# Kernel optimization log

Hardware: AMD Instinct MI355X
Metric: run time of the kernel (lower is better)

## Reference

```python
import jax, jax.numpy as jnp
import numpy as np

B, S, D, H = 4, 2048, 1024, 16
DH = D // H
NEG = -1e9


def setup_inputs() -> dict:
    key = jax.random.key(0)
    ks = jax.random.split(key, 6)
    return {
        "q_raw": jax.random.normal(ks[0], (B, S, D), jnp.float32),
        "kv_raw": jax.random.normal(ks[1], (B, S, D), jnp.float32),
        "padding_mask": jnp.ones((B, S), jnp.int32),
        "Wq": jax.random.normal(ks[2], (D, D), jnp.float32) * 0.02,
        "Wk": jax.random.normal(ks[3], (D, D), jnp.float32) * 0.02,
        "Wv": jax.random.normal(ks[4], (D, D), jnp.float32) * 0.02,
        "Wo": jax.random.normal(ks[5], (D, D), jnp.float32) * 0.02,
    }


def _split_heads(x):
    # (B, S, D) -> (B, H, S, DH)
    return x.reshape(B, S, H, DH).transpose(0, 2, 1, 3)


def reference(q_raw, kv_raw, padding_mask, Wq, Wk, Wv, Wo):
    # nn.Linear (no bias): y = x @ W.T
    q = _split_heads(q_raw @ Wq.T)
    k = _split_heads(kv_raw @ Wk.T)
    v = _split_heads(kv_raw @ Wv.T)

    scale = 1.0 / jnp.sqrt(jnp.float32(DH))
    scores = jnp.einsum("bhqd,bhkd->bhqk", q, k) * scale  # (B,H,S,S)

    # padding mask: 0 -> masked (broadcast over query dim), as in torch code
    pad = (padding_mask == 0)[:, None, None, :]  # (B,1,1,S)
    scores = jnp.where(pad, NEG, scores)
    # causal mask (only applied when padding_mask given, matching original)
    causal = jnp.triu(jnp.ones((S, S), bool), k=1)  # (S,S)
    scores = jnp.where(causal[None, None], NEG, scores)

    w = jax.nn.softmax(scores, axis=-1)
    att = jnp.einsum("bhqk,bhkd->bhqd", w, v)  # (B,H,S,DH)
    att = att.transpose(0, 2, 1, 3).reshape(B, S, D)
    return att @ Wo.T
```

## Files before the change

kernel.cpp:

```cpp
#include <hip/hip_runtime.h>
#include <stdint.h>

typedef __attribute__((ext_vector_type(8))) short  short8;
typedef __attribute__((ext_vector_type(4))) float  f32x4;
typedef __attribute__((ext_vector_type(4))) unsigned short us4;

static __device__ __forceinline__ unsigned short f2bf(float x) {
  unsigned u = __builtin_bit_cast(unsigned, x);
  u += 0x7FFFu + ((u >> 16) & 1u);
  return (unsigned short)(u >> 16);
}

static __device__ __forceinline__ unsigned cvt_pk_bf16(float lo, float hi) {
  unsigned r;
  asm("v_cvt_pk_bf16_f32 %0, %1, %2" : "=v"(r) : "v"(lo), "v"(hi));
  return r;
}

template <int CTRL>
static __device__ __forceinline__ float maxdpp(float v) {
  int o = __builtin_amdgcn_update_dpp(0, __builtin_bit_cast(int, v), CTRL, 0xf, 0xf, false);
  return fmaxf(v, __builtin_bit_cast(float, o));
}
static __device__ __forceinline__ float rowmax16(float v) {
  v = maxdpp<0xB1>(v);
  v = maxdpp<0x4E>(v);
  v = maxdpp<0x141>(v);
  v = maxdpp<0x140>(v);
  return v;
}

__global__ __launch_bounds__(256) void cvt6(const float* __restrict__ q_raw,
                                            const float* __restrict__ kv_raw,
                                            const float* __restrict__ Wq,
                                            const float* __restrict__ Wk,
                                            const float* __restrict__ Wv,
                                            const float* __restrict__ Wo,
                                            unsigned short* __restrict__ qbf,
                                            unsigned short* __restrict__ kvbf,
                                            unsigned short* __restrict__ wbf) {
  const int y = blockIdx.y;
  const float* in;
  unsigned short* out;
  int n4;
  if (y == 0)      { in = q_raw;  out = qbf;  n4 = 2097152; }
  else if (y == 1) { in = kv_raw; out = kvbf; n4 = 2097152; }
  else {
    in  = (y == 2) ? Wq : (y == 3) ? Wk : (y == 4) ? Wv : Wo;
    out = wbf + (size_t)(y - 2) * 1048576;
    n4 = 262144;
  }
  int i = blockIdx.x * 256 + threadIdx.x;
  const int stride = gridDim.x * 256;
  for (; i < n4; i += stride) {
    f32x4 v = *((const f32x4*)in + i);
    us4 o = { f2bf(v[0]), f2bf(v[1]), f2bf(v[2]), f2bf(v[3]) };
    *((us4*)out + i) = o;
  }
}

__global__ __launch_bounds__(1024) void bias_kernel(const int* __restrict__ pm,
                                                    float* __restrict__ bias,
                                                    unsigned* __restrict__ flagmask) {
  __shared__ unsigned m;
  const int b = blockIdx.x, tid = threadIdx.x;
  if (tid == 0) m = 0;
  __syncthreads();
  const int i0 = b * 2048 + tid;
  const int z0 = pm[i0], z1 = pm[i0 + 1024];
  bias[i0]        = z0 ? 0.f : -1.0e9f;
  bias[i0 + 1024] = z1 ? 0.f : -1.0e9f;
  const int wv = tid >> 6;
  unsigned long long b0 = __ballot(z0 == 0);
  unsigned long long b1 = __ballot(z1 == 0);
  if ((tid & 63) == 0) {
    unsigned bits = (b0 ? (1u << wv) : 0u) | (b1 ? (1u << (wv + 16)) : 0u);
    if (bits) atomicOr(&m, bits);
  }
  __syncthreads();
  if (tid == 0) flagmask[b] = m;
}

static __device__ __forceinline__ void g2l16(const void* g, void* l) {
  __builtin_amdgcn_global_load_lds(
      (const __attribute__((address_space(1))) void*)g,
      (__attribute__((address_space(3))) void*)l, 16, 0, 0);
}

__global__ __launch_bounds__(256) void gemm_proj(const unsigned short* __restrict__ qbf,
                                                 const unsigned short* __restrict__ kvbf,
                                                 const unsigned short* __restrict__ wbf,
                                                 unsigned short* __restrict__ Qp,
                                                 unsigned short* __restrict__ Kp,
                                                 unsigned short* __restrict__ Vtp,
                                                 float qscale) {
  __shared__ unsigned short Alds[2][4096];
  __shared__ unsigned short Blds[2][4096];
  const int tid  = threadIdx.x;
  const int lane = tid & 63;
  const int w    = tid >> 6;
  const int g    = lane >> 4;
  const int li   = lane & 15;

  const int l = blockIdx.x;
  const int xcd = l & 7, j = l >> 3;
  const int mstep = j & 7, rn = j >> 3;
  const int region = rn >> 3;
  const int n0 = (rn & 7) * 128;
  const int m0 = (xcd * 8 + mstep) * 128;
  const int wm = (w >> 1) * 64;
  const int wn = (w & 1) * 64;

  const unsigned short* A = (region == 0) ? qbf : kvbf;
  const unsigned short* W = wbf + (size_t)region * 1048576;

  int aoff[4], boff[4];
#pragma unroll
  for (int mi = 0; mi < 4; ++mi) {
    int row = wm + mi * 16 + li;
    aoff[mi] = row * 32 + (g ^ ((row >> 1) & 3)) * 8;
  }
#pragma unroll
  for (int ni = 0; ni < 4; ++ni) {
    int col = wn + ni * 16 + li;
    boff[ni] = col * 32 + (g ^ ((col >> 1) & 3)) * 8;
  }

  const int s1 = tid, s2 = 256 + tid;
  const int r1 = s1 >> 2, gc1 = (s1 & 3) ^ ((r1 >> 1) & 3);
  const int r2 = s2 >> 2, gc2 = (s2 & 3) ^ ((r2 >> 1) & 3);
  const unsigned short* gA1 = A + (size_t)(m0 + r1) * 1024 + gc1 * 8;
  const unsigned short* gA2 = A + (size_t)(m0 + r2) * 1024 + gc2 * 8;
  const unsigned short* gB1 = W + (size_t)(n0 + r1) * 1024 + gc1 * 8;
  const unsigned short* gB2 = W + (size_t)(n0 + r2) * 1024 + gc2 * 8;

  f32x4 acc[4][4] = {};

  g2l16(gA1, &Alds[0][w * 512]); g2l16(gA2, &Alds[0][2048 + w * 512]);
  g2l16(gB1, &Blds[0][w * 512]); g2l16(gB2, &Blds[0][2048 + w * 512]);
  gA1 += 32; gA2 += 32; gB1 += 32; gB2 += 32;

  int cur = 0;
#pragma unroll 1
  for (int kt = 0; kt < 32; ++kt) {
    if (kt < 31) {
      g2l16(gA1, &Alds[cur ^ 1][w * 512]); g2l16(gA2, &Alds[cur ^ 1][2048 + w * 512]);
      g2l16(gB1, &Blds[cur ^ 1][w * 512]); g2l16(gB2, &Blds[cur ^ 1][2048 + w * 512]);
      gA1 += 32; gA2 += 32; gB1 += 32; gB2 += 32;
      asm volatile("s_waitcnt vmcnt(4)" ::: "memory");
    } else {
      asm volatile("s_waitcnt vmcnt(0)" ::: "memory");
    }
    __builtin_amdgcn_s_barrier();
    short8 af[4], bf[4];
#pragma unroll
    for (int mi = 0; mi < 4; ++mi) af[mi] = *(const short8*)&Alds[cur][aoff[mi]];
#pragma unroll
    for (int ni = 0; ni < 4; ++ni) bf[ni] = *(const short8*)&Blds[cur][boff[ni]];
#pragma unroll
    for (int mi = 0; mi < 4; ++mi)
#pragma unroll
      for (int ni = 0; ni < 4; ++ni)
        acc[mi][ni] = __builtin_amdgcn_mfma_f32_16x16x32_bf16(af[mi], bf[ni], acc[mi][ni], 0, 0, 0);
    __builtin_amdgcn_s_barrier();
    cur ^= 1;
  }

  if (region == 2) {
#pragma unroll
    for (int mi = 0; mi < 4; ++mi) {
      int mb = m0 + wm + mi * 16 + g * 4;
      int bb = mb >> 11, s = mb & 2047;
#pragma unroll
      for (int ni = 0; ni < 4; ++ni) {
        int n = n0 + wn + ni * 16 + li;
        us4 pk = { f2bf(acc[mi][ni][0]), f2bf(acc[mi][ni][1]),
                   f2bf(acc[mi][ni][2]), f2bf(acc[mi][ni][3]) };
        *(us4*)&Vtp[(size_t)(bb * 1024 + n) * 2048 + s] = pk;
      }
    }
  } else {
    unsigned short* C = (region == 0) ? Qp : Kp;
    const float sc = (region == 0) ? qscale : 1.0f;
#pragma unroll
    for (int mi = 0; mi < 4; ++mi) {
      int mb = m0 + wm + mi * 16 + g * 4;
#pragma unroll
      for (int ni = 0; ni < 4; ++ni) {
        int n = n0 + wn + ni * 16 + li;
#pragma unroll
        for (int r = 0; r < 4; ++r)
          C[(size_t)(mb + r) * 1024 + n] = f2bf(acc[mi][ni][r] * sc);
      }
    }
  }
}

__global__ __launch_bounds__(256) void gemm_out(const unsigned short* __restrict__ A,
                                                const unsigned short* __restrict__ W,
                                                float* __restrict__ C) {
  __shared__ unsigned short Alds[2][4096];
  __shared__ unsigned short Blds[2][4096];
  const int tid  = threadIdx.x;
  const int lane = tid & 63;
  const int w    = tid >> 6;
  const int g    = lane >> 4;
  const int li   = lane & 15;

  const int l = blockIdx.x;
  const int xcd = l & 7, j = l >> 3;
  const int mstep = j & 7, nt = j >> 3;
  const int m0 = (xcd * 8 + mstep) * 128;
  const int n0 = nt * 128;
  const int wm = (w >> 1) * 64;
  const int wn = (w & 1) * 64;

  int aoff[4], boff[4];
#pragma unroll
  for (int mi = 0; mi < 4; ++mi) {
    int row = wm + mi * 16 + li;
    aoff[mi] = row * 32 + (g ^ ((row >> 1) & 3)) * 8;
  }
#pragma unroll
  for (int ni = 0; ni < 4; ++ni) {
    int col = wn + ni * 16 + li;
    boff[ni] = col * 32 + (g ^ ((col >> 1) & 3)) * 8;
  }

  const int s1 = tid, s2 = 256 + tid;
  const int r1 = s1 >> 2, gc1 = (s1 & 3) ^ ((r1 >> 1) & 3);
  const int r2 = s2 >> 2, gc2 = (s2 & 3) ^ ((r2 >> 1) & 3);
  const unsigned short* gA1 = A + (size_t)(m0 + r1) * 1024 + gc1 * 8;
  const unsigned short* gA2 = A + (size_t)(m0 + r2) * 1024 + gc2 * 8;
  const unsigned short* gB1 = W + (size_t)(n0 + r1) * 1024 + gc1 * 8;
  const unsigned short* gB2 = W + (size_t)(n0 + r2) * 1024 + gc2 * 8;

  f32x4 acc[4][4] = {};

  g2l16(gA1, &Alds[0][w * 512]); g2l16(gA2, &Alds[0][2048 + w * 512]);
  g2l16(gB1, &Blds[0][w * 512]); g2l16(gB2, &Blds[0][2048 + w * 512]);
  gA1 += 32; gA2 += 32; gB1 += 32; gB2 += 32;

  int cur = 0;
#pragma unroll 1
  for (int kt = 0; kt < 32; ++kt) {
    if (kt < 31) {
      g2l16(gA1, &Alds[cur ^ 1][w * 512]); g2l16(gA2, &Alds[cur ^ 1][2048 + w * 512]);
      g2l16(gB1, &Blds[cur ^ 1][w * 512]); g2l16(gB2, &Blds[cur ^ 1][2048 + w * 512]);
      gA1 += 32; gA2 += 32; gB1 += 32; gB2 += 32;
      asm volatile("s_waitcnt vmcnt(4)" ::: "memory");
    } else {
      asm volatile("s_waitcnt vmcnt(0)" ::: "memory");
    }
    __builtin_amdgcn_s_barrier();
    short8 af[4], bf[4];
#pragma unroll
    for (int mi = 0; mi < 4; ++mi) af[mi] = *(const short8*)&Alds[cur][aoff[mi]];
#pragma unroll
    for (int ni = 0; ni < 4; ++ni) bf[ni] = *(const short8*)&Blds[cur][boff[ni]];
#pragma unroll
    for (int mi = 0; mi < 4; ++mi)
#pragma unroll
      for (int ni = 0; ni < 4; ++ni)
        acc[mi][ni] = __builtin_amdgcn_mfma_f32_16x16x32_bf16(af[mi], bf[ni], acc[mi][ni], 0, 0, 0);
    __builtin_amdgcn_s_barrier();
    cur ^= 1;
  }

#pragma unroll
  for (int mi = 0; mi < 4; ++mi) {
    int mb = m0 + wm + mi * 16 + g * 4;
#pragma unroll
    for (int ni = 0; ni < 4; ++ni) {
      int n = n0 + wn + ni * 16 + li;
#pragma unroll
      for (int r = 0; r < 4; ++r)
        C[(size_t)(mb + r) * 1024 + n] = acc[mi][ni][r];
    }
  }
}

__global__ __launch_bounds__(256, 4) void attn_kernel(const unsigned short* __restrict__ Qp,
                                                      const unsigned short* __restrict__ Kp,
                                                      const unsigned short* __restrict__ Vt,
                                                      const float* __restrict__ bias,
                                                      const unsigned* __restrict__ flagmask,
                                                      unsigned short* __restrict__ att) {
  __shared__ unsigned short Klds[2][64 * 64];
  __shared__ unsigned short Vlds[2][64 * 64];
  __shared__ unsigned short Plds[4][16 * 64];

  const int tid = threadIdx.x, lane = tid & 63, w = tid >> 6;
  const int g = lane >> 4, li = lane & 15;

  const int rid = blockIdx.x + (blockIdx.y << 4);
  const int xcd = rid & 7, kk = rid >> 3;
  const int bh = (kk & 7) | (xcd << 3);
  const int b = bh >> 4, h = bh & 15;
  const int tA = kk >> 3, tB = 31 - tA;
  const int nA = tA + 1, nB = tB + 1;

  const unsigned smask = flagmask[b];

  const int s1 = tid, s2 = tid + 256;
  const int r1 = s1 >> 3, c1 = (s1 & 7) ^ (r1 & 7);
  const int r2 = s2 >> 3, c2 = (s2 & 7) ^ (r2 & 7);
  const unsigned short* Kb1 = Kp + (size_t)(b * 2048 + r1) * 1024 + h * 64 + c1 * 8;
  const unsigned short* Kb2 = Kp + (size_t)(b * 2048 + r2) * 1024 + h * 64 + c2 * 8;
  const unsigned short* Vb1 = Vt + (size_t)(b * 1024 + h * 64 + r1) * 2048 + c1 * 8;
  const unsigned short* Vb2 = Vt + (size_t)(b * 1024 + h * 64 + r2) * 2048 + c2 * 8;

  int foff[2][4];
#pragma unroll
  for (int ks = 0; ks < 2; ++ks)
#pragma unroll
    for (int i = 0; i < 4; ++i)
      foff[ks][i] = (i * 16 + li) * 64 + (((ks * 4 + g) ^ (li & 7)) * 8);

  unsigned short* Pl = &Plds[w][0];
  const int swr = (li & 7) ^ (li >> 3);
  int poff[2];
#pragma unroll
  for (int ks = 0; ks < 2; ++ks) poff[ks] = li * 64 + ((ks * 4 + g) ^ swr) * 8;

  const float* bbase = bias + b * 2048 + li;

  short8 ones;
#pragma unroll
  for (int j2 = 0; j2 < 8; ++j2) ones[j2] = (short)0x3F80;

  int qw = tA * 64 + w * 16;
  short8 qfr[2];
#pragma unroll
  for (int ks = 0; ks < 2; ++ks)
    qfr[ks] = *(const short8*)&Qp[((size_t)(b * 2048 + qw + li)) * 1024 +
                                  h * 64 + ks * 32 + g * 8];

  f32x4 acco[4] = {};
  f32x4 lacc = {};
  float mrow[4] = {-3.0e38f, -3.0e38f, -3.0e38f, -3.0e38f};
  const f32x4 Z = {0.f, 0.f, 0.f, 0.f};

  auto stage = [&](int kt, int bufn) {
    const size_t ko = (size_t)kt * 65536, vo = (size_t)kt * 64;
    g2l16(Kb1 + ko, &Klds[bufn][w * 512]);
    g2l16(Kb2 + ko, &Klds[bufn][2048 + w * 512]);
    g2l16(Vb1 + vo, &Vlds[bufn][w * 512]);
    g2l16(Vb2 + vo, &Vlds[bufn][2048 + w * 512]);
  };

  auto body = [&](int kt, bool diag, int buf) {
    f32x4 s[4];
#pragma unroll
    for (int ni = 0; ni < 4; ++ni) {
      short8 kf = *(const short8*)&Klds[buf][foff[0][ni]];
      s[ni] = __builtin_amdgcn_mfma_f32_16x16x32_bf16(qfr[0], kf, Z, 0, 0, 0);
    }
#pragma unroll
    for (int ni = 0; ni < 4; ++ni) {
      short8 kf = *(const short8*)&Klds[buf][foff[1][ni]];
      s[ni] = __builtin_amdgcn_mfma_f32_16x16x32_bf16(qfr[1], kf, s[ni], 0, 0, 0);
    }
    if ((smask >> kt) & 1u) {
#pragma unroll
      for (int ni = 0; ni < 4; ++ni) {
        float bv = bbase[kt * 64 + ni * 16];
#pragma unroll
        for (int r = 0; r < 4; ++r) s[ni][r] += bv;
      }
    }
    if (diag) {
      const int q0 = qw + g * 4;
#pragma unroll
      for (int ni = 0; ni < 4; ++ni) {
        const int key = kt * 64 + ni * 16 + li;
#pragma unroll
        for (int r = 0; r < 4; ++r)
          if (key > q0 + r) s[ni][r] = -1.0e9f;
      }
    }
    float tm[4];
#pragma unroll
    for (int r = 0; r < 4; ++r)
      tm[r] = rowmax16(fmaxf(fmaxf(s[0][r], s[1][r]), fmaxf(s[2][r], s[3][r])));
    int need = 0;
#pragma unroll
    for (int r = 0; r < 4; ++r) need |= (tm[r] > mrow[r] + 8.0f) ? 1 : 0;
    if (__any(need)) {
#pragma unroll
      for (int r = 0; r < 4; ++r) {
        const float mn = fmaxf(mrow[r], tm[r]);
        const float al = __builtin_amdgcn_exp2f(mrow[r] - mn);
        mrow[r] = mn;
        lacc[r] *= al;
#pragma unroll
        for (int df = 0; df < 4; ++df) acco[df][r] *= al;
      }
    }
#pragma unroll
    for (int ni = 0; ni < 4; ++ni) {
#pragma unroll
      for (int h2 = 0; h2 < 2; ++h2) {
        float lo = __builtin_amdgcn_exp2f(s[ni][2 * h2]     - mrow[2 * h2]);
        float hi = __builtin_amdgcn_exp2f(s[ni][2 * h2 + 1] - mrow[2 * h2 + 1]);
        unsigned pk = cvt_pk_bf16(lo, hi);
        const int r0 = g * 4 + 2 * h2;
        const int ch = 2 * ni + (li >> 3);
        const int lo7 = li & 7;
        Pl[r0 * 64 + ((ch ^ ((r0 & 7) ^ (g >> 1))) * 8) + lo7] = (unsigned short)pk;
        const int rr = r0 + 1;
        Pl[rr * 64 + ((ch ^ ((rr & 7) ^ (g >> 1))) * 8) + lo7] = (unsigned short)(pk >> 16);
      }
    }
#pragma unroll
    for (int ks = 0; ks < 2; ++ks) {
      const short8 pa = *(const short8*)&Pl[poff[ks]];
      short8 vf[4];
#pragma unroll
      for (int df = 0; df < 4; ++df) vf[df] = *(const short8*)&Vlds[buf][foff[ks][df]];
#pragma unroll
      for (int df = 0; df < 4; ++df)
        acco[df] = __builtin_amdgcn_mfma_f32_16x16x32_bf16(pa, vf[df], acco[df], 0, 0, 0);
      lacc = __builtin_amdgcn_mfma_f32_16x16x32_bf16(pa, ones, lacc, 0, 0, 0);
    }
  };

  auto epilogue = [&]() {
    float inv[4];
#pragma unroll
    for (int r = 0; r < 4; ++r) inv[r] = __builtin_amdgcn_rcpf(lacc[r]);
    const int qb0 = qw + g * 4;
#pragma unroll
    for (int df = 0; df < 4; ++df) {
      const int d = h * 64 + df * 16 + li;
#pragma unroll
      for (int r = 0; r < 4; ++r)
        att[(size_t)(b * 2048 + qb0 + r) * 1024 + d] = f2bf(acco[df][r] * inv[r]);
    }
  };

  stage(0, 0);
  int buf = 0;

#pragma unroll 1
  for (int kt = 0; kt < nA; ++kt) {
    stage((kt + 1 < nA) ? kt + 1 : 0, buf ^ 1);
    asm volatile("s_waitcnt vmcnt(4)" ::: "memory");
    __builtin_amdgcn_s_barrier();
    body(kt, kt == nA - 1, buf);
    __builtin_amdgcn_s_barrier();
    buf ^= 1;
  }

  epilogue();
  qw = tB * 64 + w * 16;
#pragma unroll
  for (int ks = 0; ks < 2; ++ks)
    qfr[ks] = *(const short8*)&Qp[((size_t)(b * 2048 + qw + li)) * 1024 +
                                  h * 64 + ks * 32 + g * 8];
#pragma unroll
  for (int df = 0; df < 4; ++df) acco[df] = Z;
  lacc = Z;
#pragma unroll
  for (int r = 0; r < 4; ++r) mrow[r] = -3.0e38f;

#pragma unroll 1
  for (int kt = 0; kt < nB; ++kt) {
    if (kt + 1 < nB) {
      stage(kt + 1, buf ^ 1);
      asm volatile("s_waitcnt vmcnt(4)" ::: "memory");
    } else {
      asm volatile("s_waitcnt vmcnt(0)" ::: "memory");
    }
    __builtin_amdgcn_s_barrier();
    body(kt, kt == nB - 1, buf);
    __builtin_amdgcn_s_barrier();
    buf ^= 1;
  }

  epilogue();
}

extern "C" void kernel_launch(void* const* d_in, const int* in_sizes, int n_in,
                              void* d_out, int out_size, void* d_ws, size_t ws_size,
                              hipStream_t stream) {
  const float* q_raw  = (const float*)d_in[0];
  const float* kv_raw = (const float*)d_in[1];
  const int*   pmask  = (const int*)d_in[2];
  const float* Wq = (const float*)d_in[3];
  const float* Wk = (const float*)d_in[4];
  const float* Wv = (const float*)d_in[5];
  const float* Wo = (const float*)d_in[6];
  float* out = (float*)d_out;

  const size_t NEL = 8388608;
  const size_t WEL = 1048576;
  unsigned short* ws   = (unsigned short*)d_ws;
  unsigned short* qbf  = ws;
  unsigned short* kvbf = qbf + NEL;
  unsigned short* wbf  = kvbf + NEL;
  unsigned short* Qp   = wbf + 4 * WEL;
  unsigned short* Kp   = Qp + NEL;
  unsigned short* Vtp  = Kp + NEL;
  float*          bias = (float*)(Vtp + NEL);
  unsigned*       flagmask = (unsigned*)(bias + 8192);
  unsigned short* att  = qbf;

  const float sc = 0.125f * 1.44269504088896340736f;

  cvt6<<<dim3(512, 6), 256, 0, stream>>>(q_raw, kv_raw, Wq, Wk, Wv, Wo, qbf, kvbf, wbf);
  bias_kernel<<<4, 1024, 0, stream>>>(pmask, bias, flagmask);
  gemm_proj<<<1536, 256, 0, stream>>>(qbf, kvbf, wbf, Qp, Kp, Vtp, sc);
  attn_kernel<<<dim3(16, 64), 256, 0, stream>>>(Qp, Kp, Vtp, bias, flagmask, att);
  gemm_out<<<512, 256, 0, stream>>>(att, wbf + 3 * WEL, out);
}
```

Before: 191.2 us.

## Compute transposed scores to keep P in registers, dropping the LDS round-trip

Swaps the MFMA operand order so the score tile comes out transposed, with each lane holding one query row and keys permuted to match the PV A-operand layout. P can then be packed straight from registers into the second MFMA, which removes the per-wave P shared-memory buffer with its scattered 16-bit stores and reloads. Row max becomes an in-lane reduction plus two cross-lane shuffles, and the rescale factor is redistributed with ds_bpermute. It also adds s_setprio around the MFMA blocks. The cost is extra permutation logic and bpermute traffic on rescale steps.

```diff
diff --git a/kernel.cpp b/kernel.cpp
--- a/kernel.cpp
+++ b/kernel.cpp
@@ -4,6 +4,7 @@
 typedef __attribute__((ext_vector_type(8))) short  short8;
 typedef __attribute__((ext_vector_type(4))) float  f32x4;
 typedef __attribute__((ext_vector_type(4))) unsigned short us4;
+typedef __attribute__((ext_vector_type(4))) unsigned int u32x4;
 
 static __device__ __forceinline__ unsigned short f2bf(float x) {
   unsigned u = __builtin_bit_cast(unsigned, x);
@@ -15,19 +16,6 @@
   unsigned r;
   asm("v_cvt_pk_bf16_f32 %0, %1, %2" : "=v"(r) : "v"(lo), "v"(hi));
   return r;
-}
-
-template <int CTRL>
-static __device__ __forceinline__ float maxdpp(float v) {
-  int o = __builtin_amdgcn_update_dpp(0, __builtin_bit_cast(int, v), CTRL, 0xf, 0xf, false);
-  return fmaxf(v, __builtin_bit_cast(float, o));
-}
-static __device__ __forceinline__ float rowmax16(float v) {
-  v = maxdpp<0xB1>(v);
-  v = maxdpp<0x4E>(v);
-  v = maxdpp<0x141>(v);
-  v = maxdpp<0x140>(v);
-  return v;
 }
 
 __global__ __launch_bounds__(256) void cvt6(const float* __restrict__ q_raw,
@@ -288,7 +276,6 @@
                                                       unsigned short* __restrict__ att) {
   __shared__ unsigned short Klds[2][64 * 64];
   __shared__ unsigned short Vlds[2][64 * 64];
-  __shared__ unsigned short Plds[4][16 * 64];
 
   const int tid = threadIdx.x, lane = tid & 63, w = tid >> 6;
   const int g = lane >> 4, li = lane & 15;
@@ -310,20 +297,18 @@
   const unsigned short* Vb1 = Vt + (size_t)(b * 1024 + h * 64 + r1) * 2048 + c1 * 8;
   const unsigned short* Vb2 = Vt + (size_t)(b * 1024 + h * 64 + r2) * 2048 + c2 * 8;
 
-  int foff[2][4];
+  int foffK[2][4], foffV[2][4];
 #pragma unroll
   for (int ks = 0; ks < 2; ++ks)
 #pragma unroll
-    for (int i = 0; i < 4; ++i)
-      foff[ks][i] = (i * 16 + li) * 64 + (((ks * 4 + g) ^ (li & 7)) * 8);
-
-  unsigned short* Pl = &Plds[w][0];
-  const int swr = (li & 7) ^ (li >> 3);
-  int poff[2];
-#pragma unroll
-  for (int ks = 0; ks < 2; ++ks) poff[ks] = li * 64 + ((ks * 4 + g) ^ swr) * 8;
-
-  const float* bbase = bias + b * 2048 + li;
+    for (int ni = 0; ni < 4; ++ni) {
+      const int krow = (ni >> 1) * 32 + (li >> 2) * 8 + (ni & 1) * 4 + (li & 3);
+      foffK[ks][ni] = krow * 64 + (((ks * 4 + g) ^ (krow & 7)) * 8);
+      const int vrow = ni * 16 + li;
+      foffV[ks][ni] = vrow * 64 + (((ks * 4 + g) ^ (vrow & 7)) * 8);
+    }
+
+  const float* bbase = bias + b * 2048 + g * 8;
 
   short8 ones;
 #pragma unroll
@@ -338,7 +323,7 @@
 
   f32x4 acco[4] = {};
   f32x4 lacc = {};
-  float mrow[4] = {-3.0e38f, -3.0e38f, -3.0e38f, -3.0e38f};
+  float m = -3.0e38f;
   const f32x4 Z = {0.f, 0.f, 0.f, 0.f};
 
   auto stage = [&](int kt, int bufn) {
@@ -351,77 +336,82 @@
 
   auto body = [&](int kt, bool diag, int buf) {
     f32x4 s[4];
+    __builtin_amdgcn_s_setprio(1);
 #pragma unroll
     for (int ni = 0; ni < 4; ++ni) {
-      short8 kf = *(const short8*)&Klds[buf][foff[0][ni]];
-      s[ni] = __builtin_amdgcn_mfma_f32_16x16x32_bf16(qfr[0], kf, Z, 0, 0, 0);
+      short8 kf = *(const short8*)&Klds[buf][foffK[0][ni]];
+      s[ni] = __builtin_amdgcn_mfma_f32_16x16x32_bf16(kf, qfr[0], Z, 0, 0, 0);
     }
 #pragma unroll
     for (int ni = 0; ni < 4; ++ni) {
-      short8 kf = *(const short8*)&Klds[buf][foff[1][ni]];
-      s[ni] = __builtin_amdgcn_mfma_f32_16x16x32_bf16(qfr[1], kf, s[ni], 0, 0, 0);
-    }
+      short8 kf = *(const short8*)&Klds[buf][foffK[1][ni]];
+      s[ni] = __builtin_amdgcn_mfma_f32_16x16x32_bf16(kf, qfr[1], s[ni], 0, 0, 0);
+    }
+    __builtin_amdgcn_s_setprio(0);
     if ((smask >> kt) & 1u) {
 #pragma unroll
       for (int ni = 0; ni < 4; ++ni) {
-        float bv = bbase[kt * 64 + ni * 16];
-#pragma unroll
-        for (int r = 0; r < 4; ++r) s[ni][r] += bv;
+        f32x4 bv = *(const f32x4*)&bbase[kt * 64 + (ni >> 1) * 32 + (ni & 1) * 4];
+#pragma unroll
+        for (int r = 0; r < 4; ++r) s[ni][r] += bv[r];
       }
     }
     if (diag) {
-      const int q0 = qw + g * 4;
+      const int q0 = qw + li;
 #pragma unroll
       for (int ni = 0; ni < 4; ++ni) {
-        const int key = kt * 64 + ni * 16 + li;
+        const int kb = kt * 64 + (ni >> 1) * 32 + g * 8 + (ni & 1) * 4;
 #pragma unroll
         for (int r = 0; r < 4; ++r)
-          if (key > q0 + r) s[ni][r] = -1.0e9f;
+          if (kb + r > q0) s[ni][r] = -1.0e9f;
       }
     }
-    float tm[4];
+    f32x4 tv;
 #pragma unroll
     for (int r = 0; r < 4; ++r)
-      tm[r] = rowmax16(fmaxf(fmaxf(s[0][r], s[1][r]), fmaxf(s[2][r], s[3][r])));
-    int need = 0;
-#pragma unroll
-    for (int r = 0; r < 4; ++r) need |= (tm[r] > mrow[r] + 8.0f) ? 1 : 0;
-    if (__any(need)) {
+      tv[r] = fmaxf(fmaxf(s[0][r], s[1][r]), fmaxf(s[2][r], s[3][r]));
+    float tm = fmaxf(fmaxf(tv[0], tv[1]), fmaxf(tv[2], tv[3]));
+    tm = fmaxf(tm, __shfl_xor(tm, 16));
+    tm = fmaxf(tm, __shfl_xor(tm, 32));
+    if (__any(tm > m + 8.0f)) {
+      const float mn = fmaxf(m, tm);
+      const float al = __builtin_amdgcn_exp2f(m - mn);
+      m = mn;
+      float alpv[4];
+#pragma unroll
+      for (int r = 0; r < 4; ++r)
+        alpv[r] = __builtin_bit_cast(float,
+            __builtin_amdgcn_ds_bpermute((g * 4 + r) * 4, __builtin_bit_cast(int, al)));
 #pragma unroll
       for (int r = 0; r < 4; ++r) {
-        const float mn = fmaxf(mrow[r], tm[r]);
-        const float al = __builtin_amdgcn_exp2f(mrow[r] - mn);
-        mrow[r] = mn;
-        lacc[r] *= al;
-#pragma unroll
-        for (int df = 0; df < 4; ++df) acco[df][r] *= al;
+        lacc[r] *= alpv[r];
+#pragma unroll
+        for (int df = 0; df < 4; ++df) acco[df][r] *= alpv[r];
       }
     }
+    unsigned wpk[4][2];
 #pragma unroll
     for (int ni = 0; ni < 4; ++ni) {
 #pragma unroll
-      for (int h2 = 0; h2 < 2; ++h2) {
-        float lo = __builtin_amdgcn_exp2f(s[ni][2 * h2]     - mrow[2 * h2]);
-        float hi = __builtin_amdgcn_exp2f(s[ni][2 * h2 + 1] - mrow[2 * h2 + 1]);
-        unsigned pk = cvt_pk_bf16(lo, hi);
-        const int r0 = g * 4 + 2 * h2;
-        const int ch = 2 * ni + (li >> 3);
-        const int lo7 = li & 7;
-        Pl[r0 * 64 + ((ch ^ ((r0 & 7) ^ (g >> 1))) * 8) + lo7] = (unsigned short)pk;
-        const int rr = r0 + 1;
-        Pl[rr * 64 + ((ch ^ ((rr & 7) ^ (g >> 1))) * 8) + lo7] = (unsigned short)(pk >> 16);
+      for (int a = 0; a < 2; ++a) {
+        float lo = __builtin_amdgcn_exp2f(s[ni][2 * a]     - m);
+        float hi = __builtin_amdgcn_exp2f(s[ni][2 * a + 1] - m);
+        wpk[ni][a] = cvt_pk_bf16(lo, hi);
       }
     }
 #pragma unroll
     for (int ks = 0; ks < 2; ++ks) {
-      const short8 pa = *(const short8*)&Pl[poff[ks]];
+      u32x4 pw = { wpk[2 * ks][0], wpk[2 * ks][1], wpk[2 * ks + 1][0], wpk[2 * ks + 1][1] };
+      const short8 pa = __builtin_bit_cast(short8, pw);
       short8 vf[4];
 #pragma unroll
-      for (int df = 0; df < 4; ++df) vf[df] = *(const short8*)&Vlds[buf][foff[ks][df]];
+      for (int df = 0; df < 4; ++df) vf[df] = *(const short8*)&Vlds[buf][foffV[ks][df]];
+      __builtin_amdgcn_s_setprio(1);
 #pragma unroll
       for (int df = 0; df < 4; ++df)
         acco[df] = __builtin_amdgcn_mfma_f32_16x16x32_bf16(pa, vf[df], acco[df], 0, 0, 0);
       lacc = __builtin_amdgcn_mfma_f32_16x16x32_bf16(pa, ones, lacc, 0, 0, 0);
+      __builtin_amdgcn_s_setprio(0);
     }
   };
 
@@ -461,8 +451,7 @@
 #pragma unroll
   for (int df = 0; df < 4; ++df) acco[df] = Z;
   lacc = Z;
-#pragma unroll
-  for (int r = 0; r < 4; ++r) mrow[r] = -3.0e38f;
+  m = -3.0e38f;
 
 #pragma unroll 1
   for (int kt = 0; kt < nB; ++kt) {
```

After: 177.4 us. -7.2%, faster.
